# Optimization experiments

Measured on AMD Instinct MI355X. Metric: run time of the kernel, lower is better.

## Reference

```python
import math
import jax, jax.numpy as jnp
import numpy as np

N_HEAD = 16

def _slopes(n_head):
    # Matches MHA_aLiBi.get_slope (static, so computed with numpy)
    cp2 = 2 ** int(math.floor(math.log2(n_head)))
    slopes = (0.5) ** np.arange(1, cp2 + 1)
    if cp2 < n_head:
        intra = 1.0 / math.sqrt(2.0)
        pair = intra ** np.arange(1, 1 + 2 * (n_head - cp2), 2)
        slopes = np.sort(np.concatenate([slopes, pair]))[::-1]
    return jnp.asarray(slopes, dtype=jnp.float32)  # [H]

def _alibi_bias(S):
    # bias[i,j] = -(i-j) for i>=j, 0 for i<j
    d = jnp.arange(S)[:, None] - jnp.arange(S)[None, :]
    return -jnp.maximum(d, 0).astype(jnp.float32)  # [S,S]

def setup_inputs() -> dict:
    key = jax.random.key(0)
    B, S, D = 2, 2048, 1024
    ks = jax.random.split(key, 12)
    f = lambda k, sh: jax.random.normal(k, sh, dtype=jnp.float32)
    inp = {
        "q": f(ks[0], (B, S, D)),
        "k": f(ks[1], (B, S, D)),
        "v": f(ks[2], (B, S, D)),
        "mask": jnp.tril(jnp.ones((S, S), dtype=jnp.int32))[None, None],  # causal [1,1,S,S]
        "wq_w": f(ks[3], (D, D)) * 0.02, "wq_b": f(ks[4], (D,)) * 0.02,
        "wk_w": f(ks[5], (D, D)) * 0.02, "wk_b": f(ks[6], (D,)) * 0.02,
        "wv_w": f(ks[7], (D, D)) * 0.02, "wv_b": f(ks[8], (D,)) * 0.02,
        "out_w": f(ks[9], (D, D)) * 0.02, "out_b": f(ks[10], (D,)) * 0.02,
    }
    return inp

def reference(q, k, v, mask, wq_w, wq_b, wk_w, wk_b, wv_w, wv_b, out_w, out_b):
    B, S, D = q.shape
    H = N_HEAD
    hd = D // H
    lin = lambda x, w, b: x @ w.T + b  # torch nn.Linear
    # project and split heads: [B,S,D] -> [B,H,S,hd]
    split = lambda x: x.reshape(B, S, H, hd).transpose(0, 2, 1, 3)
    wq = split(lin(q, wq_w, wq_b))
    wk = split(lin(k, wk_w, wk_b))
    wv = split(lin(v, wv_w, wv_b))
    qk = jnp.einsum("bhsd,bhtd->bhst", wq, wk)  # [B,H,S,S] (no 1/sqrt(d) scaling, per source)
    alibi = _alibi_bias(S)[None, :, :] * _slopes(H)[:, None, None]  # [H,S,S]
    attn = qk + alibi[None]
    attn = jnp.where(mask == 0, jnp.float32(-1e9), attn)
    attn = jax.nn.softmax(attn, axis=-1)
    out = jnp.einsum("bhst,bhtd->bhsd", attn, wv)
    out = out.transpose(0, 2, 1, 3).reshape(B, S, D)
    return lin(out, out_w, out_b)
```

## Files before the change

kernel.cpp:

```cpp
#include <hip/hip_runtime.h>
#include <hip/hip_bf16.h>
#include <cstdint>
#include <cstddef>

#define DEV static __device__ __forceinline__

typedef float f32x4 __attribute__((ext_vector_type(4)));
typedef __bf16 bf16x8 __attribute__((ext_vector_type(8)));
typedef __bf16 bf16x4 __attribute__((ext_vector_type(4)));

#define EXP2F(x) __builtin_amdgcn_exp2f(x)

union B8 {
  uint4 u4;
  uint32_t u[4];
  unsigned short s[8];
  bf16x8 v;
};
union B4 {
  uint2 u2;
  unsigned short s[4];
  bf16x4 v;
};

DEV unsigned short bfbits(float x) {
  union { __bf16 h; unsigned short s; } z; z.h = (__bf16)x; return z.s;
}
DEV uint32_t pk2(float x, float y) {
  union { __bf16 h[2]; uint32_t u; } z;
  z.h[0] = (__bf16)x; z.h[1] = (__bf16)y; return z.u;
}

DEV f32x4 mfma_bf16(bf16x8 a, bf16x8 b, f32x4 c) {
  return __builtin_amdgcn_mfma_f32_16x16x32_bf16(a, b, c, 0, 0, 0);
}

DEV void gload16(const void* g, void* l) {
  __builtin_amdgcn_global_load_lds(
      (const __attribute__((address_space(1))) void*)g,
      (__attribute__((address_space(3))) void*)l, 16, 0, 0);
}

__global__ __launch_bounds__(256)
void cvt_all(const float* __restrict__ q, const float* __restrict__ k,
             const float* __restrict__ v,
             const float* __restrict__ wq, const float* __restrict__ wk,
             const float* __restrict__ wv, const float* __restrict__ ow,
             unsigned short* __restrict__ dst) {
  const int bid = blockIdx.x;
  const size_t base = ((size_t)bid << 11) + ((size_t)threadIdx.x << 3);
  const float* src;
  size_t rel;
  if (bid < 2048)      { src = q; rel = base; }
  else if (bid < 4096) { src = k; rel = base - (1u << 22); }
  else if (bid < 6144) { src = v; rel = base - (2u << 22); }
  else {
    const int wseg = (bid - 6144) >> 9;
    src = wseg == 0 ? wq : wseg == 1 ? wk : wseg == 2 ? wv : ow;
    rel = base & 1048575u;
  }
  float4 a0 = *(const float4*)(src + rel);
  float4 a1 = *(const float4*)(src + rel + 4);
  B8 p;
  p.u[0] = pk2(a0.x, a0.y); p.u[1] = pk2(a0.z, a0.w);
  p.u[2] = pk2(a1.x, a1.y); p.u[3] = pk2(a1.z, a1.w);
  *(uint4*)(dst + base) = p.u4;
}

__global__ __launch_bounds__(256, 2)
void gemm_qkv_b(const unsigned short* __restrict__ qb,
                const unsigned short* __restrict__ kb,
                const unsigned short* __restrict__ vb,
                const unsigned short* __restrict__ wqb,
                const unsigned short* __restrict__ wkb,
                const unsigned short* __restrict__ wvb,
                const float* __restrict__ bq, const float* __restrict__ bk,
                const float* __restrict__ bv,
                unsigned short* __restrict__ Qp, unsigned short* __restrict__ Kp,
                unsigned short* __restrict__ Vt) {
  const int K = 1024, N = 1024;
  __shared__ __align__(16) unsigned short As[128 * 64];
  __shared__ __align__(16) unsigned short Bs[128 * 64];
  const int bid = blockIdx.x;
  const int lbid = (bid & 7) * 96 + (bid >> 3);
  const int proj = lbid >> 8;
  const int t = lbid & 255;
  const int mb = t >> 3, nb = t & 7;
  const unsigned short* A  = proj == 0 ? qb  : proj == 1 ? kb  : vb;
  const unsigned short* Bw = proj == 0 ? wqb : proj == 1 ? wkb : wvb;
  const float* bias        = proj == 0 ? bq  : proj == 1 ? bk  : bv;
  const int tid = threadIdx.x;
  const int lane = tid & 63, w = tid >> 6;
  const int wm = w >> 1, wn = w & 1;
  f32x4 acc[4][4] = {};

  const int lrow = lane >> 3;
  const int lg = lane & 7;
  const int gsrc = lg ^ lrow;
  const unsigned short* ag = A  + (size_t)(mb * 128 + w * 32 + lrow) * K + gsrc * 8;
  const unsigned short* bg = Bw + (size_t)(nb * 128 + w * 32 + lrow) * K + gsrc * 8;
  unsigned short* al = &As[(w * 32) * 64];
  unsigned short* bl = &Bs[(w * 32) * 64];

  for (int kt = 0; kt < 16; ++kt) {
    __syncthreads();
#pragma unroll
    for (int i = 0; i < 4; ++i) {
      gload16(ag + i * (8 * 1024) + kt * 64, al + (i * 8) * 64);
      gload16(bg + i * (8 * 1024) + kt * 64, bl + (i * 8) * 64);
    }
    __syncthreads();

    B8 af[4][2], bfr[4][2];
#pragma unroll
    for (int mi = 0; mi < 4; ++mi)
#pragma unroll
      for (int kk = 0; kk < 2; ++kk) {
        const int row = wm * 64 + mi * 16 + (lane & 15);
        const int slot = ((kk << 2) + (lane >> 4)) ^ (row & 7);
        af[mi][kk].u4 = *(const uint4*)&As[(row << 6) + (slot << 3)];
      }
#pragma unroll
    for (int ni = 0; ni < 4; ++ni)
#pragma unroll
      for (int kk = 0; kk < 2; ++kk) {
        const int row = wn * 64 + ni * 16 + (lane & 15);
        const int slot = ((kk << 2) + (lane >> 4)) ^ (row & 7);
        bfr[ni][kk].u4 = *(const uint4*)&Bs[(row << 6) + (slot << 3)];
      }
#pragma unroll
    for (int kk = 0; kk < 2; ++kk)
#pragma unroll
      for (int mi = 0; mi < 4; ++mi)
#pragma unroll
        for (int ni = 0; ni < 4; ++ni)
          acc[mi][ni] = mfma_bf16(af[mi][kk].v, bfr[ni][kk].v, acc[mi][ni]);
  }

  unsigned short* Cv = proj == 0 ? Qp : proj == 1 ? Kp : Vt;
  const bool vt_mode = (proj == 2);
#pragma unroll
  for (int ni = 0; ni < 4; ++ni) {
    const int col = nb * 128 + wn * 64 + ni * 16 + (lane & 15);
    const float bv = bias[col];
#pragma unroll
    for (int mi = 0; mi < 4; ++mi) {
#pragma unroll
      for (int r = 0; r < 4; ++r) {
        const int row = mb * 128 + wm * 64 + mi * 16 + (lane >> 4) * 4 + r;
        const float val = acc[mi][ni][r] + bv;
        if (!vt_mode) {
          Cv[(size_t)row * N + col] = bfbits(val);
        } else {
          const int b = row >> 11, ss = row & 2047, hh = col >> 6, d = col & 63;
          Cv[((size_t)((b * 16 + hh) * 64 + d) << 11) + ss] = bfbits(val);
        }
      }
    }
  }
}

__global__ __launch_bounds__(256, 2)
void gemm_out_b(const unsigned short* __restrict__ At,
                const unsigned short* __restrict__ wob,
                const float* __restrict__ bias, float* __restrict__ Cv) {
  const int K = 1024, N = 1024;
  __shared__ __align__(16) unsigned short As[64 * 64];
  __shared__ __align__(16) unsigned short Bs[128 * 64];
  const int bid = blockIdx.x;
  const int lbid = (bid & 7) * 64 + (bid >> 3);
  const int mb = lbid >> 3, nb = lbid & 7;
  const int tid = threadIdx.x;
  const int lane = tid & 63, w = tid >> 6;
  const int qc = lane & 15, g = lane >> 4;
  f32x4 acc[4][2] = {};

  const int lrow = lane >> 3, lg = lane & 7;
  const int gsrc = lg ^ lrow;
  const unsigned short* ag = At  + (size_t)(mb * 64 + w * 16 + lrow) * K + gsrc * 8;
  const unsigned short* bg = wob + (size_t)(nb * 128 + w * 32 + lrow) * K + gsrc * 8;
  unsigned short* al = &As[(w * 16) * 64];
  unsigned short* bl = &Bs[(w * 32) * 64];

  for (int kt = 0; kt < 16; ++kt) {
    __syncthreads();
#pragma unroll
    for (int i = 0; i < 2; ++i)
      gload16(ag + i * (8 * 1024) + kt * 64, al + (i * 8) * 64);
#pragma unroll
    for (int i = 0; i < 4; ++i)
      gload16(bg + i * (8 * 1024) + kt * 64, bl + (i * 8) * 64);
    __syncthreads();

    B8 af[4][2], bfr[2][2];
#pragma unroll
    for (int mi = 0; mi < 4; ++mi)
#pragma unroll
      for (int kk = 0; kk < 2; ++kk) {
        const int row = mi * 16 + qc;
        const int slot = ((kk << 2) + g) ^ (row & 7);
        af[mi][kk].u4 = *(const uint4*)&As[(row << 6) + (slot << 3)];
      }
#pragma unroll
    for (int ni = 0; ni < 2; ++ni)
#pragma unroll
      for (int kk = 0; kk < 2; ++kk) {
        const int row = w * 32 + ni * 16 + qc;
        const int slot = ((kk << 2) + g) ^ (row & 7);
        bfr[ni][kk].u4 = *(const uint4*)&Bs[(row << 6) + (slot << 3)];
      }
#pragma unroll
    for (int kk = 0; kk < 2; ++kk)
#pragma unroll
      for (int mi = 0; mi < 4; ++mi)
#pragma unroll
        for (int ni = 0; ni < 2; ++ni)
          acc[mi][ni] = mfma_bf16(af[mi][kk].v, bfr[ni][kk].v, acc[mi][ni]);
  }

#pragma unroll
  for (int ni = 0; ni < 2; ++ni) {
    const int col = nb * 128 + w * 32 + ni * 16 + qc;
    const float bv = bias[col];
#pragma unroll
    for (int mi = 0; mi < 4; ++mi) {
#pragma unroll
      for (int r = 0; r < 4; ++r) {
        const int row = mb * 64 + mi * 16 + g * 4 + r;
        Cv[(size_t)row * N + col] = acc[mi][ni][r] + bv;
      }
    }
  }
}

__global__ __launch_bounds__(256, 4)
void flash_alibi(const unsigned short* __restrict__ Qp,
                 const unsigned short* __restrict__ Kp,
                 const unsigned short* __restrict__ Vt,
                 unsigned short* __restrict__ At) {
  const int S = 2048, Dm = 1024;
  const int bid0 = blockIdx.x;
  const int lbid = (bid0 & 7) * 128 + (bid0 >> 3);
  const int z = lbid >> 5, y = lbid & 31;
  const int s = ((8 * (y & 3)) + (y >> 2) + 8 * (z & 3) + (z >> 2)) & 31;
  const int h = z & 15, b = z >> 4;
  const int tid = threadIdx.x, lane = tid & 63, w = tid >> 6;
  const int qc = lane & 15, g = lane >> 4;
  const int q0 = s * 64 + w * 16;
  const int qcol = q0 + qc;
  const float slope = exp2f(-(float)(h + 1));
  const float L2E = 1.44269504f;
  const float ls1 = L2E * slope;
  const float THR = 11.54f;
  const size_t bS = (size_t)b * S;
  const int hoff = h * 64;
  const int ntile = s + 1;

  __shared__ __align__(16) unsigned short Ks[64 * 64];
  __shared__ __align__(16) unsigned short Vs[64 * 64];

  B8 qf[2];
  {
    const unsigned short* qa = Qp + (bS + qcol) * Dm + hoff + g * 8;
    qf[0].u4 = *(const uint4*)qa; qf[1].u4 = *(const uint4*)(qa + 32);
  }

  const int q7 = qc & 7;
  const int gk0 = g ^ q7;
  const int gk1 = gk0 ^ 4;
  const int krow = w * 16 + qc;
  const unsigned short* kgA = Kp + (bS + krow) * Dm + hoff + g * 8;
  const unsigned short* kgB = Kp + (bS + krow) * Dm + hoff + (g ^ 4) * 8;
  const unsigned short* vgA =
      Vt + (((size_t)((b * 16 + h) * 64 + krow)) << 11) + g * 8;
  const unsigned short* vgB =
      Vt + (((size_t)((b * 16 + h) * 64 + krow)) << 11) + (g ^ 4) * 8;
  unsigned short* kwA = &Ks[krow * 64 + gk0 * 8];
  unsigned short* kwB = &Ks[krow * 64 + gk1 * 8];
  unsigned short* vwA = &Vs[krow * 64 + gk0 * 8];
  unsigned short* vwB = &Vs[krow * 64 + gk1 * 8];
  uint4 krA, krB, vrA, vrB;

#define SLOAD(TT) do {                                                         \
    const size_t ko_ = ((size_t)(TT) << 6) * Dm;                               \
    krA = *(const uint4*)(kgA + ko_); krB = *(const uint4*)(kgB + ko_);        \
    vrA = *(const uint4*)(vgA + ((TT) << 6));                                  \
    vrB = *(const uint4*)(vgB + ((TT) << 6));                                  \
  } while (0)
#define SWRITE() do {                                                          \
    *(uint4*)kwA = krA; *(uint4*)kwB = krB;                                    \
    *(uint4*)vwA = vrA; *(uint4*)vwB = vrB;                                    \
  } while (0)

  const int sw = qc & 7;
  const unsigned short* krd0 = &Ks[qc * 64 + ((g ^ sw) << 3)];
  const unsigned short* krd1 = &Ks[qc * 64 + (((g ^ sw) ^ 4) << 3)];
  const unsigned short* vrd[4];
#pragma unroll
  for (int j = 0; j < 4; ++j)
    vrd[j] = &Vs[qc * 64 + ((((2 * j) + (g >> 1)) ^ sw) << 3) + (g & 1) * 4];

  f32x4 acc[4] = {};
  float m_run = 0.f, l_run = 0.f;
  const float abq = slope * (float)(g * 4 - qcol);

#define FRAGX(KV0, MASKED) do {                                                \
    const float kv0f = (float)(KV0);                                           \
    f32x4 sc_[4] = {};                                                         \
    _Pragma("unroll")                                                          \
    for (int f_ = 0; f_ < 4; ++f_) {                                           \
      B8 k0_, k1_;                                                             \
      k0_.u4 = *(const uint4*)(krd0 + f_ * 1024);                              \
      k1_.u4 = *(const uint4*)(krd1 + f_ * 1024);                              \
      sc_[f_] = mfma_bf16(k0_.v, qf[0].v, sc_[f_]);                            \
      sc_[f_] = mfma_bf16(k1_.v, qf[1].v, sc_[f_]);                            \
    }                                                                          \
    const float cb_ = (fmaf(slope, kv0f, abq) - m_run) * L2E;                  \
    float ein_[4][4]; float emax_ = -1e30f;                                    \
    _Pragma("unroll")                                                          \
    for (int f_ = 0; f_ < 4; ++f_) {                                           \
      const float cf_ = cb_ + (float)(16 * f_) * ls1;                          \
      _Pragma("unroll")                                                        \
      for (int r_ = 0; r_ < 4; ++r_) {                                         \
        float e_ = fmaf(sc_[f_][r_], L2E, cf_ + (float)r_ * ls1);              \
        if (MASKED) {                                                          \
          const int kv_ = (KV0) + f_ * 16 + g * 4 + r_;                        \
          if (kv_ > qcol) e_ = -1e30f;                                         \
        }                                                                      \
        ein_[f_][r_] = e_; emax_ = fmaxf(emax_, e_);                           \
      }                                                                        \
    }                                                                          \
    if (!__all(emax_ <= THR)) {                                                \
      float er_ = fmaxf(emax_, __shfl_xor(emax_, 16));                         \
      er_ = fmaxf(er_, __shfl_xor(er_, 32));                                   \
      er_ = fmaxf(er_, 0.f);                                                   \
      m_run += er_ * 0.69314718f;                                              \
      const float sfac_ = EXP2F(-er_);                                         \
      l_run *= sfac_;                                                          \
      _Pragma("unroll") for (int n_ = 0; n_ < 4; ++n_) acc[n_] = acc[n_] * sfac_; \
      _Pragma("unroll") for (int f_ = 0; f_ < 4; ++f_)                         \
        _Pragma("unroll") for (int r_ = 0; r_ < 4; ++r_) ein_[f_][r_] -= er_;  \
    }                                                                          \
    B8 pf0_, pf1_; float lsum_ = 0.f;                                          \
    _Pragma("unroll")                                                          \
    for (int f_ = 0; f_ < 4; ++f_) {                                           \
      _Pragma("unroll")                                                        \
      for (int r_ = 0; r_ < 4; ++r_) {                                         \
        const float p_ = EXP2F(ein_[f_][r_]);                                  \
        lsum_ += p_;                                                           \
        if (f_ == 0)      pf0_.v[r_]     = (__bf16)p_;                         \
        else if (f_ == 1) pf0_.v[4 + r_] = (__bf16)p_;                         \
        else if (f_ == 2) pf1_.v[r_]     = (__bf16)p_;                         \
        else              pf1_.v[4 + r_] = (__bf16)p_;                         \
      }                                                                        \
    }                                                                          \
    l_run += lsum_;                                                            \
    _Pragma("unroll")                                                          \
    for (int n_ = 0; n_ < 4; ++n_) {                                           \
      B8 v0_, v1_;                                                             \
      uint2 a0_ = *(const uint2*)(vrd[0] + n_ * 1024);                         \
      uint2 a1_ = *(const uint2*)(vrd[1] + n_ * 1024);                         \
      uint2 a2_ = *(const uint2*)(vrd[2] + n_ * 1024);                         \
      uint2 a3_ = *(const uint2*)(vrd[3] + n_ * 1024);                         \
      v0_.u[0] = a0_.x; v0_.u[1] = a0_.y;                                      \
      v0_.u[2] = a1_.x; v0_.u[3] = a1_.y;                                      \
      v1_.u[0] = a2_.x; v1_.u[1] = a2_.y;                                      \
      v1_.u[2] = a3_.x; v1_.u[3] = a3_.y;                                      \
      acc[n_] = mfma_bf16(v0_.v, pf0_.v, acc[n_]);                             \
      acc[n_] = mfma_bf16(v1_.v, pf1_.v, acc[n_]);                             \
    }                                                                          \
  } while (0)

  SLOAD(0);
  SWRITE();
  __syncthreads();

  for (int t = 0; t < ntile - 1; ++t) {
    SLOAD(t + 1);
    FRAGX(t << 6, 0);
    __syncthreads();
    SWRITE();
    __syncthreads();
  }
  FRAGX((ntile - 1) << 6, 1);

  float lt = l_run + __shfl_xor(l_run, 16);
  lt += __shfl_xor(lt, 32);
  const float ri = 1.0f / lt;
  unsigned short* ob = At + (bS + qcol) * Dm + hoff;
#pragma unroll
  for (int n = 0; n < 4; ++n) {
    B4 ov;
    ov.v[0] = (__bf16)(acc[n][0] * ri);
    ov.v[1] = (__bf16)(acc[n][1] * ri);
    ov.v[2] = (__bf16)(acc[n][2] * ri);
    ov.v[3] = (__bf16)(acc[n][3] * ri);
    *(uint2*)(ob + n * 16 + g * 4) = ov.u2;
  }
}

extern "C" void kernel_launch(void* const* d_in, const int* in_sizes, int n_in,
                              void* d_out, int out_size, void* d_ws, size_t ws_size,
                              hipStream_t stream) {
  const float* q    = (const float*)d_in[0];
  const float* k    = (const float*)d_in[1];
  const float* v    = (const float*)d_in[2];
  const float* wq_w = (const float*)d_in[4];
  const float* wq_b = (const float*)d_in[5];
  const float* wk_w = (const float*)d_in[6];
  const float* wk_b = (const float*)d_in[7];
  const float* wv_w = (const float*)d_in[8];
  const float* wv_b = (const float*)d_in[9];
  const float* ow   = (const float*)d_in[10];
  const float* ob   = (const float*)d_in[11];
  float* out = (float*)d_out;

  char* ws = (char*)d_ws;
  unsigned short* Qp = (unsigned short*)(ws);
  unsigned short* Kp = (unsigned short*)(ws + (8u << 20));
  unsigned short* Vt = (unsigned short*)(ws + (16u << 20));
  unsigned short* At = (unsigned short*)(ws + (24u << 20));
  unsigned short* cvt = (unsigned short*)(ws + (32u << 20));
  unsigned short* qb  = cvt;
  unsigned short* kb  = cvt + (1u << 22);
  unsigned short* vb  = cvt + (2u << 22);
  unsigned short* wqb = cvt + (3u << 22);
  unsigned short* wkb = wqb + (1u << 20);
  unsigned short* wvb = wkb + (1u << 20);
  unsigned short* wob = wvb + (1u << 20);

  dim3 blk(256);
  cvt_all<<<8192, blk, 0, stream>>>(q, k, v, wq_w, wk_w, wv_w, ow, cvt);
  gemm_qkv_b<<<768, blk, 0, stream>>>(qb, kb, vb, wqb, wkb, wvb,
                                      wq_b, wk_b, wv_b, Qp, Kp, Vt);
  flash_alibi<<<1024, blk, 0, stream>>>(Qp, Kp, Vt, At);
  gemm_out_b<<<512, blk, 0, stream>>>(At, wob, ob, out);
}
```

Baseline: 123.9 us.

## Stage 128-key K/V tiles per barrier pair in flash attention

The attention kernel now loads two 64-key K and V tiles into doubled shared-memory buffers per iteration and processes both halves before synchronising, which halves the number of __syncthreads pairs and global-load rounds. The tail handles odd or even query-block counts by masking only the last 64-key half. This doubles LDS usage and register staging (eight uint4 prefetch registers), which may reduce occupancy, and for even s the last staged tile loads a partially unused block.

```diff
diff --git a/kernel.cpp b/kernel.cpp
--- a/kernel.cpp
+++ b/kernel.cpp
@@ -254,10 +254,10 @@
   const float THR = 11.54f;
   const size_t bS = (size_t)b * S;
   const int hoff = h * 64;
-  const int ntile = s + 1;
-
-  __shared__ __align__(16) unsigned short Ks[64 * 64];
-  __shared__ __align__(16) unsigned short Vs[64 * 64];
+  const int T = (s + 2) >> 1;
+
+  __shared__ __align__(16) unsigned short Ks[128 * 64];
+  __shared__ __align__(16) unsigned short Vs[64 * 128];
 
   B8 qf[2];
   {
@@ -271,47 +271,55 @@
   const int krow = w * 16 + qc;
   const unsigned short* kgA = Kp + (bS + krow) * Dm + hoff + g * 8;
   const unsigned short* kgB = Kp + (bS + krow) * Dm + hoff + (g ^ 4) * 8;
-  const unsigned short* vgA =
-      Vt + (((size_t)((b * 16 + h) * 64 + krow)) << 11) + g * 8;
-  const unsigned short* vgB =
-      Vt + (((size_t)((b * 16 + h) * 64 + krow)) << 11) + (g ^ 4) * 8;
+  const unsigned short* vg0 =
+      Vt + (((size_t)((b * 16 + h) * 64 + krow)) << 11);
   unsigned short* kwA = &Ks[krow * 64 + gk0 * 8];
   unsigned short* kwB = &Ks[krow * 64 + gk1 * 8];
-  unsigned short* vwA = &Vs[krow * 64 + gk0 * 8];
-  unsigned short* vwB = &Vs[krow * 64 + gk1 * 8];
-  uint4 krA, krB, vrA, vrB;
+  unsigned short* vwA = &Vs[krow * 128 + gk0 * 8];
+  unsigned short* vwB = &Vs[krow * 128 + gk1 * 8];
+  uint4 kr0, kr1, kr2, kr3, vr0, vr1, vr2, vr3;
 
 #define SLOAD(TT) do {                                                         \
-    const size_t ko_ = ((size_t)(TT) << 6) * Dm;                               \
-    krA = *(const uint4*)(kgA + ko_); krB = *(const uint4*)(kgB + ko_);        \
-    vrA = *(const uint4*)(vgA + ((TT) << 6));                                  \
-    vrB = *(const uint4*)(vgB + ((TT) << 6));                                  \
+    const size_t ko_ = ((size_t)(TT) << 7) * Dm;                               \
+    kr0 = *(const uint4*)(kgA + ko_);                                          \
+    kr1 = *(const uint4*)(kgB + ko_);                                          \
+    kr2 = *(const uint4*)(kgA + ko_ + (size_t)64 * Dm);                        \
+    kr3 = *(const uint4*)(kgB + ko_ + (size_t)64 * Dm);                        \
+    const int vo_ = (TT) << 7;                                                 \
+    vr0 = *(const uint4*)(vg0 + vo_ + g * 8);                                  \
+    vr1 = *(const uint4*)(vg0 + vo_ + (g ^ 4) * 8);                            \
+    vr2 = *(const uint4*)(vg0 + vo_ + 64 + g * 8);                             \
+    vr3 = *(const uint4*)(vg0 + vo_ + 64 + (g ^ 4) * 8);                       \
   } while (0)
 #define SWRITE() do {                                                          \
-    *(uint4*)kwA = krA; *(uint4*)kwB = krB;                                    \
-    *(uint4*)vwA = vrA; *(uint4*)vwB = vrB;                                    \
+    *(uint4*)kwA = kr0; *(uint4*)kwB = kr1;                                    \
+    *(uint4*)(kwA + 64 * 64) = kr2; *(uint4*)(kwB + 64 * 64) = kr3;            \
+    *(uint4*)vwA = vr0; *(uint4*)vwB = vr1;                                    \
+    *(uint4*)(vwA + 64) = vr2; *(uint4*)(vwB + 64) = vr3;                      \
   } while (0)
 
-  const int sw = qc & 7;
-  const unsigned short* krd0 = &Ks[qc * 64 + ((g ^ sw) << 3)];
-  const unsigned short* krd1 = &Ks[qc * 64 + (((g ^ sw) ^ 4) << 3)];
-  const unsigned short* vrd[4];
-#pragma unroll
-  for (int j = 0; j < 4; ++j)
-    vrd[j] = &Vs[qc * 64 + ((((2 * j) + (g >> 1)) ^ sw) << 3) + (g & 1) * 4];
+  const unsigned short* krd0 = &Ks[qc * 64 + ((g ^ q7)) * 8];
+  const unsigned short* krd1 = &Ks[qc * 64 + (((g ^ 4) ^ q7)) * 8];
+  const unsigned short* vrdA[4];
+  const unsigned short* vrdB[4];
+#pragma unroll
+  for (int j = 0; j < 4; ++j) {
+    vrdA[j] = &Vs[qc * 128 + (((2 * j) + (g >> 1)) ^ q7) * 8 + (g & 1) * 4];
+    vrdB[j] = &Vs[qc * 128 + ((8 + (2 * j) + (g >> 1)) ^ q7) * 8 + (g & 1) * 4];
+  }
 
   f32x4 acc[4] = {};
   float m_run = 0.f, l_run = 0.f;
   const float abq = slope * (float)(g * 4 - qcol);
 
-#define FRAGX(KV0, MASKED) do {                                                \
+#define FRAGX(KV0, HL, MASKED) do {                                            \
     const float kv0f = (float)(KV0);                                           \
     f32x4 sc_[4] = {};                                                         \
     _Pragma("unroll")                                                          \
     for (int f_ = 0; f_ < 4; ++f_) {                                           \
       B8 k0_, k1_;                                                             \
-      k0_.u4 = *(const uint4*)(krd0 + f_ * 1024);                              \
-      k1_.u4 = *(const uint4*)(krd1 + f_ * 1024);                              \
+      k0_.u4 = *(const uint4*)(krd0 + (HL) * 4096 + f_ * 1024);                \
+      k1_.u4 = *(const uint4*)(krd1 + (HL) * 4096 + f_ * 1024);                \
       sc_[f_] = mfma_bf16(k0_.v, qf[0].v, sc_[f_]);                            \
       sc_[f_] = mfma_bf16(k1_.v, qf[1].v, sc_[f_]);                            \
     }                                                                          \
@@ -355,13 +363,14 @@
       }                                                                        \
     }                                                                          \
     l_run += lsum_;                                                            \
+    const unsigned short* const* vrd_ = (HL) ? vrdB : vrdA;                    \
     _Pragma("unroll")                                                          \
     for (int n_ = 0; n_ < 4; ++n_) {                                           \
       B8 v0_, v1_;                                                             \
-      uint2 a0_ = *(const uint2*)(vrd[0] + n_ * 1024);                         \
-      uint2 a1_ = *(const uint2*)(vrd[1] + n_ * 1024);                         \
-      uint2 a2_ = *(const uint2*)(vrd[2] + n_ * 1024);                         \
-      uint2 a3_ = *(const uint2*)(vrd[3] + n_ * 1024);                         \
+      uint2 a0_ = *(const uint2*)(vrd_[0] + n_ * 2048);                        \
+      uint2 a1_ = *(const uint2*)(vrd_[1] + n_ * 2048);                        \
+      uint2 a2_ = *(const uint2*)(vrd_[2] + n_ * 2048);                        \
+      uint2 a3_ = *(const uint2*)(vrd_[3] + n_ * 2048);                        \
       v0_.u[0] = a0_.x; v0_.u[1] = a0_.y;                                      \
       v0_.u[2] = a1_.x; v0_.u[3] = a1_.y;                                      \
       v1_.u[0] = a2_.x; v1_.u[1] = a2_.y;                                      \
@@ -375,14 +384,23 @@
   SWRITE();
   __syncthreads();
 
-  for (int t = 0; t < ntile - 1; ++t) {
+  for (int t = 0; t < T - 1; ++t) {
     SLOAD(t + 1);
-    FRAGX(t << 6, 0);
+    FRAGX((t << 7), 0, 0);
+    FRAGX((t << 7) + 64, 1, 0);
     __syncthreads();
     SWRITE();
     __syncthreads();
   }
-  FRAGX((ntile - 1) << 6, 1);
+  {
+    const int kv0l = (T - 1) << 7;
+    if (s & 1) {
+      FRAGX(kv0l, 0, 0);
+      FRAGX(kv0l + 64, 1, 1);
+    } else {
+      FRAGX(kv0l, 0, 1);
+    }
+  }
 
   float lt = l_run + __shfl_xor(l_run, 16);
   lt += __shfl_xor(lt, 32);
```

Measured after the change: 127.9 us. 1.03x slower.
